# Optimization experiments

Hardware: AMD Instinct MI355X
Metric: run time of the kernel (lower is better)

Reference implementation:

```python
import jax, jax.numpy as jnp
import numpy as np

DIM = 128
WS = 16

def conv2d(x, w, b, padding=0, dilation=1, groups=1):
    out = jax.lax.conv_general_dilated(
        x, w, (1, 1), [(padding, padding), (padding, padding)],
        rhs_dilation=(dilation, dilation),
        dimension_numbers=('NCHW', 'OIHW', 'NCHW'),
        feature_group_count=groups)
    return out + b[None, :, None, None]

def leaky(x):
    return jax.nn.leaky_relu(x, 0.2)

def to_windows(x, ws):
    # [B,C,H,W] -> [B, N, ws*ws*C]  with per-window (dh, dw, c) flatten order
    B, C, H, W = x.shape
    h, w = H // ws, W // ws
    return x.reshape(B, C, h, ws, w, ws).transpose(0, 2, 4, 3, 5, 1).reshape(B, h * w, ws * ws * C)

def from_windows(x, ws, h, w, C):
    B = x.shape[0]
    return x.reshape(B, h, w, ws, ws, C).transpose(0, 5, 1, 3, 2, 4).reshape(B, C, h * ws, w * ws)

def flow_warp(x, flow):
    # bilinear warp with border padding; flow [B,H,W,2] in pixel units (x,y)
    B, C, H, W = x.shape
    gy, gx = jnp.meshgrid(jnp.arange(H, dtype=x.dtype), jnp.arange(W, dtype=x.dtype), indexing='ij')
    sx = jnp.clip(gx[None] + flow[..., 0], 0.0, W - 1.0)
    sy = jnp.clip(gy[None] + flow[..., 1], 0.0, H - 1.0)
    x0 = jnp.floor(sx); y0 = jnp.floor(sy)
    x1 = jnp.clip(x0 + 1.0, 0.0, W - 1.0); y1 = jnp.clip(y0 + 1.0, 0.0, H - 1.0)
    wx = (sx - x0)[:, None]; wy = (sy - y0)[:, None]
    x0i = x0.astype(jnp.int32); x1i = x1.astype(jnp.int32)
    y0i = y0.astype(jnp.int32); y1i = y1.astype(jnp.int32)
    gat = jax.vmap(lambda img, yi, xi: img[:, yi, xi])
    Ia = gat(x, y0i, x0i); Ib = gat(x, y0i, x1i)
    Ic = gat(x, y1i, x0i); Id = gat(x, y1i, x1i)
    return Ia * (1 - wx) * (1 - wy) + Ib * wx * (1 - wy) + Ic * (1 - wx) * wy + Id * wx * wy

def _forward(x, condition_global, gumbel_u, pv_w, pv_b, pq_w, pq_b, pk_w, pk_b,
             cs1_w, cs1_b, cs2_w, cs2_b, cs3_w, cs3_b, po_w, po_b,
             rin_w, rin_b, roff1_w, roff1_b, roff2_w, roff2_b,
             rm1_w, rm1_b, rm2_w, rm2_b, rca_w, rca_b, rsa_w, rsa_b):
    B, C, H, W = x.shape
    ws = WS
    v = conv2d(x, pv_w, pv_b)
    # window coordinate condition, 2 channels
    lin = jnp.linspace(-1.0, 1.0, ws).astype(x.dtype)
    cy, cx = jnp.meshgrid(lin, lin, indexing='ij')
    cond_wind = jnp.tile(jnp.stack([cy, cx])[None], (B, 1, H // ws, W // ws))
    cond = jnp.concatenate([v, condition_global, cond_wind], axis=1)  # [B, C+3, H, W]
    # PredictorLG
    f = leaky(conv2d(cond, rin_w, rin_b))
    offsets = conv2d(leaky(conv2d(f, roff1_w, roff1_b)), roff2_w, roff2_b)  # [B,2,H,W]
    ca = jax.nn.sigmoid(conv2d(f.mean(axis=(2, 3), keepdims=True), rca_w, rca_b))  # [B,C,1,1]
    sa = jax.nn.sigmoid(conv2d(f, rsa_w, rsa_b, padding=1))  # [B,1,H,W]
    mwin = to_windows(f.mean(axis=1, keepdims=True), ws)  # [B,N,ws*ws]
    h1 = leaky(jnp.einsum('bne,oe->bno', mwin, rm1_w) + rm1_b)
    pred = jax.nn.softmax(jnp.einsum('bne,oe->bno', h1, rm2_w) + rm2_b, axis=-1)  # [B,N,2]
    # hard gumbel-softmax with straight-through estimator (tau=1)
    g = -jnp.log(-jnp.log(gumbel_u + 1e-10) + 1e-10)
    y_soft = jax.nn.softmax(pred + g, axis=-1)
    y_hard = jax.nn.one_hot(jnp.argmax(y_soft, -1), 2, dtype=y_soft.dtype)
    mask = (y_hard + y_soft - jax.lax.stop_gradient(y_soft))[:, :, 0:1]  # [B,N,1]
    # flow warp, q=k=warped
    xw = flow_warp(x, offsets.transpose(0, 2, 3, 1))
    qk = jnp.concatenate([xw, xw], axis=1)
    vs = v * sa
    vw = to_windows(v, ws); vsw = to_windows(vs, ws); qkw = to_windows(qk, ws)
    N = vw.shape[1]
    v1 = (vw * mask).reshape(B * N, ws * ws, C)
    v2 = vsw * (1.0 - mask)
    qk1 = (qkw * mask).reshape(B, N * ws * ws, 2 * C)
    q1, k1 = jnp.split(qk1, 2, axis=2)
    q1 = (q1 @ pq_w.T + pq_b).reshape(B * N, ws * ws, C)
    k1 = (k1 @ pk_w.T + pk_b).reshape(B * N, ws * ws, C)
    attn = jax.nn.softmax(q1 @ jnp.swapaxes(k1, -1, -2), axis=-1)  # [B*N, ws^2, ws^2]
    f_attn = (attn @ v1).reshape(B, N, ws * ws * C)
    out = from_windows(f_attn + v2, ws, H // ws, W // ws, C)
    cs = conv2d(out, cs1_w, cs1_b)
    cs = conv2d(cs, cs2_w, cs2_b, padding=2, groups=C)
    cs = conv2d(cs, cs3_w, cs3_b, padding=6, dilation=3, groups=C)
    out = jax.nn.gelu(cs, approximate=False) * ca + out
    return conv2d(out, po_w, po_b)

def setup_inputs() -> dict:
    B, C, H, W, ws = 4, DIM, 256, 256, WS
    cdim = C + 3; c4 = cdim // 4; c8 = cdim // 8
    N = (H // ws) * (W // ws)
    ks = jax.random.split(jax.random.key(0), 20)
    s = 0.05
    def rn(k, shape, scale):
        return jax.random.normal(k, shape, dtype=jnp.float32) * scale
    z = lambda n: jnp.zeros((n,), dtype=jnp.float32)
    return {
        'x': rn(ks[0], (B, C, H, W), 1.0),
        'condition_global': rn(ks[1], (B, 1, H, W), 1.0),
        'gumbel_u': jax.random.uniform(ks[2], (B, N, 2), dtype=jnp.float32, minval=1e-6, maxval=1.0 - 1e-6),
        'pv_w': rn(ks[3], (C, C, 1, 1), s), 'pv_b': z(C),
        'pq_w': rn(ks[4], (C, C), s), 'pq_b': z(C),
        'pk_w': rn(ks[5], (C, C), s), 'pk_b': z(C),
        'cs1_w': rn(ks[6], (C, C, 1, 1), s), 'cs1_b': z(C),
        'cs2_w': rn(ks[7], (C, 1, 5, 5), s), 'cs2_b': z(C),
        'cs3_w': rn(ks[8], (C, 1, 5, 5), s), 'cs3_b': z(C),
        'po_w': rn(ks[9], (C, C, 1, 1), s), 'po_b': z(C),
        'rin_w': rn(ks[10], (c4, cdim, 1, 1), s), 'rin_b': z(c4),
        'roff1_w': rn(ks[11], (c8, c4, 1, 1), s), 'roff1_b': z(c8),
        'roff2_w': rn(ks[12], (2, c8, 1, 1), s), 'roff2_b': z(2),
        'rm1_w': rn(ks[13], (ws, ws * ws), s), 'rm1_b': z(ws),
        'rm2_w': rn(ks[14], (2, ws), s), 'rm2_b': z(2),
        'rca_w': rn(ks[15], (C, c4, 1, 1), s), 'rca_b': z(C),
        'rsa_w': rn(ks[16], (1, c4, 3, 3), s), 'rsa_b': z(1),
    }

def reference(x, condition_global, gumbel_u, pv_w, pv_b, pq_w, pq_b, pk_w, pk_b,
              cs1_w, cs1_b, cs2_w, cs2_b, cs3_w, cs3_b, po_w, po_b,
              rin_w, rin_b, roff1_w, roff1_b, roff2_w, roff2_b,
              rm1_w, rm1_b, rm2_w, rm2_b, rca_w, rca_b, rsa_w, rsa_b):
    return _forward(x, condition_global, gumbel_u, pv_w, pv_b, pq_w, pq_b, pk_w, pk_b,
                    cs1_w, cs1_b, cs2_w, cs2_b, cs3_w, cs3_b, po_w, po_b,
                    rin_w, rin_b, roff1_w, roff1_b, roff2_w, roff2_b,
                    rm1_w, rm1_b, rm2_w, rm2_b, rca_w, rca_b, rsa_w, rsa_b)
```

## Files before the change

### kernel.cpp

```cpp
#include <hip/hip_runtime.h>
#include <hip/hip_bf16.h>


typedef __hip_bfloat16 bf16;
using short8 = __attribute__((ext_vector_type(8))) short;
using f32x4  = __attribute__((ext_vector_type(4))) float;

#define HWP 65536
#define NB  4
#define LB  __launch_bounds__(256)

__device__ __forceinline__ float u2f(unsigned short s) {
    return __uint_as_float(((unsigned int)s) << 16);
}
__device__ __forceinline__ float b2f(bf16 v) { return __bfloat162float(v); }
__device__ __forceinline__ unsigned short f2bu(float x) {
    bf16 h = __float2bfloat16(x);
    return *reinterpret_cast<unsigned short*>(&h);
}
__device__ __forceinline__ float leaky(float x) { return x > 0.f ? x : 0.2f * x; }
__device__ __forceinline__ float sigmoidf(float x) { return 1.f / (1.f + __expf(-x)); }

struct __attribute__((aligned(4))) f2u { float x, y; };

__device__ __forceinline__ void ld8(const float* p, float* f) {
    float4 u0 = *reinterpret_cast<const float4*>(p);
    float4 u1 = *reinterpret_cast<const float4*>(p + 4);
    f[0] = u0.x; f[1] = u0.y; f[2] = u0.z; f[3] = u0.w;
    f[4] = u1.x; f[5] = u1.y; f[6] = u1.z; f[7] = u1.w;
}
__device__ __forceinline__ void ld8(const bf16* p, float* f) {
    uint4 u = *reinterpret_cast<const uint4*>(p);
    const unsigned short* s = reinterpret_cast<const unsigned short*>(&u);
#pragma unroll
    for (int i = 0; i < 8; i++) f[i] = u2f(s[i]);
}
__device__ __forceinline__ void st8(bf16* p, const float* f) {
    uint4 r;
    r.x = (unsigned)f2bu(f[0]) | ((unsigned)f2bu(f[1]) << 16);
    r.y = (unsigned)f2bu(f[2]) | ((unsigned)f2bu(f[3]) << 16);
    r.z = (unsigned)f2bu(f[4]) | ((unsigned)f2bu(f[5]) << 16);
    r.w = (unsigned)f2bu(f[6]) | ((unsigned)f2bu(f[7]) << 16);
    *reinterpret_cast<uint4*>(p) = r;
}
__device__ __forceinline__ void stv4(float* p, float a, float b, float c, float d) {
    float4 v; v.x = a; v.y = b; v.z = c; v.w = d;
    *reinterpret_cast<float4*>(p) = v;
}
__device__ __forceinline__ void stv4(bf16* p, float a, float b, float c, float d) {
    uint2 r;
    r.x = (unsigned)f2bu(a) | ((unsigned)f2bu(b) << 16);
    r.y = (unsigned)f2bu(c) | ((unsigned)f2bu(d) << 16);
    *reinterpret_cast<uint2*>(p) = r;
}

__global__ LB void k_pvconv(const float* __restrict__ in, const float* __restrict__ w,
                            const float* __restrict__ bias, float* __restrict__ out) {
    __shared__ float Wt[32][128];
    __shared__ float Xs[32][64];
    const int tid = threadIdx.x;
    const int p0 = blockIdx.x * 64;
    const int b = blockIdx.y;
    const int pg = tid & 15;
    const int og = tid >> 4;
    float acc[4][8];
#pragma unroll
    for (int i = 0; i < 4; i++)
#pragma unroll
        for (int j = 0; j < 8; j++) acc[i][j] = 0.f;
    const float* inb = in + ((size_t)b * 128) * HWP + p0;
    for (int k0 = 0; k0 < 128; k0 += 32) {
        __syncthreads();
#pragma unroll
        for (int it = 0; it < 4; it++) {
            int jj = tid + it * 256;
            int oc = jj & 127, kq = jj >> 7;
            float4 wv = *reinterpret_cast<const float4*>(w + oc * 128 + k0 + kq * 4);
            Wt[kq * 4 + 0][oc] = wv.x;
            Wt[kq * 4 + 1][oc] = wv.y;
            Wt[kq * 4 + 2][oc] = wv.z;
            Wt[kq * 4 + 3][oc] = wv.w;
        }
        {
            int row = tid >> 3;
            int col0 = (tid & 7) * 8;
            float t8[8];
            ld8(inb + (size_t)(k0 + row) * HWP + col0, t8);
#pragma unroll
            for (int i = 0; i < 8; i++) Xs[row][col0 + i] = t8[i];
        }
        __syncthreads();
#pragma unroll
        for (int kk = 0; kk < 32; kk++) {
            float a0 = Xs[kk][pg * 4 + 0];
            float a1 = Xs[kk][pg * 4 + 1];
            float a2 = Xs[kk][pg * 4 + 2];
            float a3 = Xs[kk][pg * 4 + 3];
            const float* wr = &Wt[kk][og * 8];
#pragma unroll
            for (int j = 0; j < 8; j++) {
                float wv = wr[j];
                acc[0][j] += a0 * wv;
                acc[1][j] += a1 * wv;
                acc[2][j] += a2 * wv;
                acc[3][j] += a3 * wv;
            }
        }
    }
#pragma unroll
    for (int j = 0; j < 8; j++) {
        int oc = og * 8 + j;
        float bv = bias[oc];
        float* po = out + ((size_t)(b * 128 + oc)) * HWP + p0 + pg * 4;
        stv4(po, acc[0][j] + bv, acc[1][j] + bv, acc[2][j] + bv, acc[3][j] + bv);
    }
}

__global__ LB void k_rin(const float* __restrict__ v, const float* __restrict__ cg,
                         const float* __restrict__ w, const float* __restrict__ bias,
                         float* __restrict__ f) {
    __shared__ float Wl[131][36];
    __shared__ float Bs[32];
    const int tid = threadIdx.x;
    for (int i = tid; i < 131 * 32; i += 256) {
        int ic = i >> 5, oc = i & 31;
        Wl[ic][oc] = w[oc * 131 + ic];
    }
    if (tid < 32) Bs[tid] = bias[tid];
    __syncthreads();
    const int p = blockIdx.x * 256 + tid;
    const int b = blockIdx.y;
    float acc[32];
#pragma unroll
    for (int o = 0; o < 32; o++) acc[o] = 0.f;
    const float* vb = v + ((size_t)b * 128) * HWP + p;
    for (int ic = 0; ic < 128; ic++) {
        float a = vb[(size_t)ic * HWP];
#pragma unroll
        for (int o = 0; o < 32; o++) acc[o] += a * Wl[ic][o];
    }
    float a128 = cg[(size_t)b * HWP + p];
    int y = p >> 8, x = p & 255;
    float a129 = -1.f + (2.f / 15.f) * (float)(y & 15);
    float a130 = -1.f + (2.f / 15.f) * (float)(x & 15);
#pragma unroll
    for (int o = 0; o < 32; o++) {
        float r = acc[o] + a128 * Wl[128][o] + a129 * Wl[129][o] + a130 * Wl[130][o] + Bs[o];
        f[((size_t)(b * 32 + o)) * HWP + p] = leaky(r);
    }
}

__global__ LB void k_offsets(const float* __restrict__ f, const float* __restrict__ w1,
                             const float* __restrict__ b1, const float* __restrict__ w2,
                             const float* __restrict__ b2, float* __restrict__ offs) {
    __shared__ float W1[32][16];
    __shared__ float W2[16][2];
    __shared__ float B1[16];
    __shared__ float B2[2];
    const int tid = threadIdx.x;
    for (int i = tid; i < 512; i += 256) {
        int ic = i >> 4, o = i & 15;
        W1[ic][o] = w1[o * 32 + ic];
    }
    if (tid < 32) { int h = tid >> 1, o = tid & 1; W2[h][o] = w2[o * 16 + h]; }
    if (tid < 16) B1[tid] = b1[tid];
    if (tid < 2) B2[tid] = b2[tid];
    __syncthreads();
    const int p = blockIdx.x * 256 + tid;
    const int b = blockIdx.y;
    float h[16];
#pragma unroll
    for (int o = 0; o < 16; o++) h[o] = B1[o];
    for (int ic = 0; ic < 32; ic++) {
        float a = f[((size_t)(b * 32 + ic)) * HWP + p];
#pragma unroll
        for (int o = 0; o < 16; o++) h[o] += a * W1[ic][o];
    }
    float o0 = B2[0], o1 = B2[1];
#pragma unroll
    for (int o = 0; o < 16; o++) {
        float hv = leaky(h[o]);
        o0 += hv * W2[o][0];
        o1 += hv * W2[o][1];
    }
    offs[((size_t)(b * 2 + 0)) * HWP + p] = o0;
    offs[((size_t)(b * 2 + 1)) * HWP + p] = o1;
}

__global__ LB void k_fpix(const float* __restrict__ f, float* __restrict__ fpix) {
    const int p = blockIdx.x * 256 + threadIdx.x;
    const int b = blockIdx.y;
    float s = 0.f;
    for (int c = 0; c < 32; c++) s += f[((size_t)(b * 32 + c)) * HWP + p];
    fpix[(size_t)b * HWP + p] = s * (1.f / 32.f);
}

__global__ LB void k_fmean(const float* __restrict__ f, float* __restrict__ fmean) {
    const int b = blockIdx.x >> 5, c = blockIdx.x & 31;
    const float* base = f + ((size_t)(b * 32 + c)) * HWP;
    float s = 0.f;
    for (int i = threadIdx.x; i < HWP; i += 256) s += base[i];
    __shared__ float red[256];
    red[threadIdx.x] = s;
    __syncthreads();
    for (int st = 128; st > 0; st >>= 1) {
        if (threadIdx.x < st) red[threadIdx.x] += red[threadIdx.x + st];
        __syncthreads();
    }
    if (threadIdx.x == 0) fmean[b * 32 + c] = red[0];
}

__global__ LB void k_ca(const float* __restrict__ fmean, const float* __restrict__ w,
                        const float* __restrict__ bias, float* __restrict__ ca) {
    const int b = blockIdx.x, oc = threadIdx.x;
    float acc = bias[oc];
    for (int ic = 0; ic < 32; ic++)
        acc += w[oc * 32 + ic] * fmean[b * 32 + ic] * (1.f / 65536.f);
    ca[b * 128 + oc] = sigmoidf(acc);
}

__global__ LB void k_sa(const float* __restrict__ f, const float* __restrict__ w,
                        const float* __restrict__ bias, float* __restrict__ sa) {
    __shared__ float Wl[32][9];
    __shared__ float bs;
    const int tid = threadIdx.x;
    for (int i = tid; i < 288; i += 256) Wl[i / 9][i % 9] = w[i];
    if (tid == 0) bs = bias[0];
    __syncthreads();
    const int p = blockIdx.x * 256 + tid;
    const int b = blockIdx.y;
    const int y = p >> 8, x = p & 255;
    float acc = bs;
    for (int ic = 0; ic < 32; ic++) {
        const float* fb = f + ((size_t)(b * 32 + ic)) * HWP;
#pragma unroll
        for (int dy = 0; dy < 3; dy++) {
            int yy = y + dy - 1;
            if ((unsigned)yy >= 256u) continue;
#pragma unroll
            for (int dx = 0; dx < 3; dx++) {
                int xx = x + dx - 1;
                if ((unsigned)xx >= 256u) continue;
                acc += fb[yy * 256 + xx] * Wl[ic][dy * 3 + dx];
            }
        }
    }
    sa[(size_t)b * HWP + p] = sigmoidf(acc);
}

__global__ LB void k_mask(const float* __restrict__ fpix, const float* __restrict__ gum,
                          const float* __restrict__ w1, const float* __restrict__ b1,
                          const float* __restrict__ w2, const float* __restrict__ b2,
                          float* __restrict__ mask) {
    __shared__ float W1[256][16];
    __shared__ float W2[2][16];
    __shared__ float B1[16];
    __shared__ float B2[2];
    const int tid = threadIdx.x;
    for (int i = tid; i < 4096; i += 256) {
        int o = i >> 8, e = i & 255;
        W1[e][o] = w1[o * 256 + e];
    }
    if (tid < 32) W2[tid >> 4][tid & 15] = w2[tid];
    if (tid < 16) B1[tid] = b1[tid];
    if (tid < 2) B2[tid] = b2[tid];
    __syncthreads();
    const int wid = blockIdx.x * 256 + tid;
    const int b = wid >> 8, n = wid & 255;
    const int wy = n >> 4, wx = n & 15;
    const float* fp = fpix + (size_t)b * HWP + (wy * 16) * 256 + wx * 16;
    float h[16];
#pragma unroll
    for (int o = 0; o < 16; o++) h[o] = B1[o];
    for (int e = 0; e < 256; e++) {
        float mv = fp[(e >> 4) * 256 + (e & 15)];
#pragma unroll
        for (int o = 0; o < 16; o++) h[o] += mv * W1[e][o];
    }
    float l0 = B2[0], l1 = B2[1];
#pragma unroll
    for (int o = 0; o < 16; o++) {
        float hv = leaky(h[o]);
        l0 += hv * W2[0][o];
        l1 += hv * W2[1][o];
    }
    float mx = fmaxf(l0, l1);
    float e0 = __expf(l0 - mx), e1 = __expf(l1 - mx);
    float inv = 1.f / (e0 + e1);
    float p0 = e0 * inv, p1 = e1 * inv;
    float u0 = gum[wid * 2 + 0], u1 = gum[wid * 2 + 1];
    float g0 = -logf(-logf(u0 + 1e-10f) + 1e-10f);
    float g1 = -logf(-logf(u1 + 1e-10f) + 1e-10f);
    mask[wid] = (p0 + g0 >= p1 + g1) ? 1.f : 0.f;
}

__global__ LB void k_warp(const float* __restrict__ x, const float* __restrict__ offs,
                          bf16* __restrict__ xw) {
    const int tid = threadIdx.x;
    const int p = blockIdx.x * 64 + (tid & 63);
    const int oct = blockIdx.y * 4 + (tid >> 6);
    const int b = blockIdx.z;
    const int y = p >> 8, xc = p & 255;
    float fx = offs[((size_t)(b * 2 + 0)) * HWP + p];
    float fy = offs[((size_t)(b * 2 + 1)) * HWP + p];
    float sx = fminf(fmaxf((float)xc + fx, 0.f), 255.f);
    float sy = fminf(fmaxf((float)y + fy, 0.f), 255.f);
    int x0 = min((int)sx, 254);
    int y0 = min((int)sy, 254);
    float wx = sx - (float)x0;
    float wy = sy - (float)y0;
    float w00 = (1.f - wx) * (1.f - wy), w01 = wx * (1.f - wy);
    float w10 = (1.f - wx) * wy, w11 = wx * wy;
    const float* base = x + ((size_t)(b * 128 + oct * 8)) * HWP + y0 * 256 + x0;
    float fv[8];
#pragma unroll
    for (int j = 0; j < 8; j++) {
        f2u r0 = *reinterpret_cast<const f2u*>(base + (size_t)j * HWP);
        f2u r1 = *reinterpret_cast<const f2u*>(base + (size_t)j * HWP + 256);
        fv[j] = r0.x * w00 + r0.y * w01 + r1.x * w10 + r1.y * w11;
    }
    const int wid = b * 256 + (y >> 4) * 16 + (xc >> 4);
    const int t = (y & 15) * 16 + (xc & 15);
    st8(xw + ((size_t)(wid * 256 + t)) * 128 + oct * 8, fv);
}

template <int MODE, typename OutT>
__global__ __launch_bounds__(256, 1) void k_wingemm(
        const bf16* __restrict__ A, const float* __restrict__ w,
        const float* __restrict__ bias, const float* __restrict__ mask,
        OutT* __restrict__ outp) {
    const int wid = blockIdx.x;
    if (MODE == 0) {
        if (mask[wid] < 0.5f) return;
    }
    __shared__ unsigned short Wl[128][136];
    __shared__ float Bs[128];
    const int tid = threadIdx.x;
    for (int j = tid; j < 4096; j += 256) {
        int oc = j >> 5, k4 = (j & 31) * 4;
        float4 wv = *reinterpret_cast<const float4*>(w + oc * 128 + k4);
        uint2 r;
        r.x = (unsigned)f2bu(wv.x) | ((unsigned)f2bu(wv.y) << 16);
        r.y = (unsigned)f2bu(wv.z) | ((unsigned)f2bu(wv.w) << 16);
        *reinterpret_cast<uint2*>(&Wl[oc][k4]) = r;
    }
    if (tid < 128) Bs[tid] = bias[tid];
    const int wv_ = tid >> 6, lane = tid & 63, quad = lane >> 4, lid = lane & 15;
    const bf16* arow = A + (size_t)wid * 256 * 128;
    short8 af[4][4];
#pragma unroll
    for (int mt = 0; mt < 4; mt++)
#pragma unroll
        for (int kf = 0; kf < 4; kf++)
            af[mt][kf] = *reinterpret_cast<const short8*>(
                arow + (size_t)(wv_ * 64 + mt * 16 + lid) * 128 + kf * 32 + quad * 8);
    __syncthreads();
    f32x4 acc[4][8];
#pragma unroll
    for (int mt = 0; mt < 4; mt++)
#pragma unroll
        for (int cf = 0; cf < 8; cf++)
#pragma unroll
            for (int i = 0; i < 4; i++) acc[mt][cf][i] = 0.f;
#pragma unroll
    for (int cf = 0; cf < 8; cf++) {
        short8 wf[4];
#pragma unroll
        for (int kf = 0; kf < 4; kf++)
            wf[kf] = *reinterpret_cast<const short8*>(&Wl[cf * 16 + lid][kf * 32 + quad * 8]);
#pragma unroll
        for (int mt = 0; mt < 4; mt++)
#pragma unroll
            for (int kf = 0; kf < 4; kf++)
                acc[mt][cf] = __builtin_amdgcn_mfma_f32_16x16x32_bf16(af[mt][kf], wf[kf], acc[mt][cf], 0, 0, 0);
    }
    if (MODE == 0) {
        bf16* ob = (bf16*)outp;
#pragma unroll
        for (int cf = 0; cf < 8; cf++) {
            float bv = Bs[cf * 16 + lid];
#pragma unroll
            for (int mt = 0; mt < 4; mt++)
#pragma unroll
                for (int i = 0; i < 4; i++) {
                    int row = wv_ * 64 + mt * 16 + quad * 4 + i;
                    *reinterpret_cast<unsigned short*>(
                        &ob[((size_t)(wid * 256 + row)) * 128 + cf * 16 + lid]) =
                        f2bu(acc[mt][cf][i] + bv);
                }
        }
    } else {
        const int b = wid >> 8, n = wid & 255;
        const int wy = n >> 4, wx = n & 15;
#pragma unroll
        for (int cf = 0; cf < 8; cf++) {
            int oc = cf * 16 + lid;
            float bv = Bs[oc];
            OutT* plane = outp + ((size_t)(b * 128 + oc)) * HWP;
#pragma unroll
            for (int mt = 0; mt < 4; mt++) {
                int t0 = wv_ * 64 + mt * 16 + quad * 4;
                int ty = t0 >> 4, tx = t0 & 15;
                int px = (wy * 16 + ty) * 256 + wx * 16 + tx;
                stv4(plane + px, acc[mt][cf][0] + bv, acc[mt][cf][1] + bv,
                     acc[mt][cf][2] + bv, acc[mt][cf][3] + bv);
            }
        }
    }
}

__global__ __launch_bounds__(256, 1) void k_attn(
        const bf16* __restrict__ qbuf, const bf16* __restrict__ kbuf,
        const float* __restrict__ v, const float* __restrict__ sa,
        const float* __restrict__ mask, bf16* __restrict__ wout) {
    const int wid = blockIdx.x;
    const int b = wid >> 8, n = wid & 255;
    const int wy = n >> 4, wx = n & 15;
    const int tid = threadIdx.x;
    const int pixbase = (wy * 16) * 256 + wx * 16;
    const float* vb = v + ((size_t)b * 128) * HWP;
    if (mask[wid] < 0.5f) {
        const int t = tid;
        const int pix = pixbase + (t >> 4) * 256 + (t & 15);
        float s = sa[(size_t)b * HWP + pix];
        bf16* orow = wout + ((size_t)(wid * 256 + t)) * 128;
        for (int c0 = 0; c0 < 128; c0 += 8) {
            float fv[8];
#pragma unroll
            for (int i = 0; i < 8; i++) fv[i] = vb[(size_t)(c0 + i) * HWP + pix] * s;
            st8(orow + c0, fv);
        }
        return;
    }
    __shared__ unsigned short Pl[4][64][72];
    __shared__ unsigned short Vt[128][72];
    const int w = tid >> 6, lane = tid & 63, quad = lane >> 4, lid = lane & 15;
    const bf16* qwin = qbuf + (size_t)wid * 256 * 128;
    const bf16* kwin = kbuf + (size_t)wid * 256 * 128;
    short8 qf[4][4];
#pragma unroll
    for (int mt = 0; mt < 4; mt++)
#pragma unroll
        for (int kf = 0; kf < 4; kf++)
            qf[mt][kf] = *reinterpret_cast<const short8*>(
                qwin + (size_t)(w * 64 + mt * 16 + lid) * 128 + kf * 32 + quad * 8);

    f32x4 O[4][8];
#pragma unroll
    for (int mt = 0; mt < 4; mt++)
#pragma unroll
        for (int cf = 0; cf < 8; cf++)
#pragma unroll
            for (int i = 0; i < 4; i++) O[mt][cf][i] = 0.f;
    float mrow[4][4], lrow[4][4];
#pragma unroll
    for (int mt = 0; mt < 4; mt++)
#pragma unroll
        for (int i = 0; i < 4; i++) { mrow[mt][i] = -1e30f; lrow[mt][i] = 0.f; }

    for (int j0 = 0; j0 < 256; j0 += 64) {
        __syncthreads();
        {
            int c = tid >> 1, jh = (tid & 1) * 32;
            const float* vcol = vb + (size_t)c * HWP + pixbase;
#pragma unroll
            for (int jj = 0; jj < 32; jj += 2) {
                int t1 = j0 + jh + jj, t2 = t1 + 1;
                float v1 = vcol[(t1 >> 4) * 256 + (t1 & 15)];
                float v2 = vcol[(t2 >> 4) * 256 + (t2 & 15)];
                unsigned u = (unsigned)f2bu(v1) | ((unsigned)f2bu(v2) << 16);
                *reinterpret_cast<unsigned*>(&Vt[c][jh + jj]) = u;
            }
        }
        f32x4 sacc[4][4];
#pragma unroll
        for (int nt = 0; nt < 4; nt++) {
            short8 kfr[4];
#pragma unroll
            for (int kf = 0; kf < 4; kf++)
                kfr[kf] = *reinterpret_cast<const short8*>(
                    kwin + (size_t)(j0 + nt * 16 + lid) * 128 + kf * 32 + quad * 8);
#pragma unroll
            for (int mt = 0; mt < 4; mt++) {
                f32x4 acc;
                acc[0] = 0.f; acc[1] = 0.f; acc[2] = 0.f; acc[3] = 0.f;
#pragma unroll
                for (int kf = 0; kf < 4; kf++)
                    acc = __builtin_amdgcn_mfma_f32_16x16x32_bf16(qf[mt][kf], kfr[kf], acc, 0, 0, 0);
                sacc[mt][nt] = acc;
            }
        }
        float alpha[4][4];
#pragma unroll
        for (int mt = 0; mt < 4; mt++)
#pragma unroll
            for (int i = 0; i < 4; i++) {
                float mx = sacc[mt][0][i];
                mx = fmaxf(mx, sacc[mt][1][i]);
                mx = fmaxf(mx, sacc[mt][2][i]);
                mx = fmaxf(mx, sacc[mt][3][i]);
                mx = fmaxf(mx, __shfl_xor(mx, 1));
                mx = fmaxf(mx, __shfl_xor(mx, 2));
                mx = fmaxf(mx, __shfl_xor(mx, 4));
                mx = fmaxf(mx, __shfl_xor(mx, 8));
                float mn = fmaxf(mrow[mt][i], mx);
                alpha[mt][i] = __expf(mrow[mt][i] - mn);
                mrow[mt][i] = mn;
            }
#pragma unroll
        for (int mt = 0; mt < 4; mt++) {
            float ps[4] = {0.f, 0.f, 0.f, 0.f};
#pragma unroll
            for (int nt = 0; nt < 4; nt++)
#pragma unroll
                for (int i = 0; i < 4; i++) {
                    float p = __expf(sacc[mt][nt][i] - mrow[mt][i]);
                    ps[i] += p;
                    Pl[w][mt * 16 + quad * 4 + i][nt * 16 + lid] = f2bu(p);
                }
#pragma unroll
            for (int i = 0; i < 4; i++) {
                float rs = ps[i];
                rs += __shfl_xor(rs, 1);
                rs += __shfl_xor(rs, 2);
                rs += __shfl_xor(rs, 4);
                rs += __shfl_xor(rs, 8);
                lrow[mt][i] = lrow[mt][i] * alpha[mt][i] + rs;
            }
        }
#pragma unroll
        for (int mt = 0; mt < 4; mt++)
#pragma unroll
            for (int cf = 0; cf < 8; cf++)
#pragma unroll
                for (int i = 0; i < 4; i++) O[mt][cf][i] *= alpha[mt][i];
        __syncthreads();
        short8 pa[4][2];
#pragma unroll
        for (int mt = 0; mt < 4; mt++)
#pragma unroll
            for (int kq = 0; kq < 2; kq++)
                pa[mt][kq] = *reinterpret_cast<const short8*>(
                    &Pl[w][mt * 16 + lid][kq * 32 + quad * 8]);
#pragma unroll
        for (int cf = 0; cf < 8; cf++) {
            short8 vf0 = *reinterpret_cast<const short8*>(&Vt[cf * 16 + lid][quad * 8]);
            short8 vf1 = *reinterpret_cast<const short8*>(&Vt[cf * 16 + lid][32 + quad * 8]);
#pragma unroll
            for (int mt = 0; mt < 4; mt++) {
                O[mt][cf] = __builtin_amdgcn_mfma_f32_16x16x32_bf16(pa[mt][0], vf0, O[mt][cf], 0, 0, 0);
                O[mt][cf] = __builtin_amdgcn_mfma_f32_16x16x32_bf16(pa[mt][1], vf1, O[mt][cf], 0, 0, 0);
            }
        }
    }
#pragma unroll
    for (int mt = 0; mt < 4; mt++) {
        float inv[4];
#pragma unroll
        for (int i = 0; i < 4; i++) inv[i] = 1.f / lrow[mt][i];
#pragma unroll
        for (int cf = 0; cf < 8; cf++)
#pragma unroll
            for (int i = 0; i < 4; i++) {
                int row = w * 64 + mt * 16 + quad * 4 + i;
                int col = cf * 16 + lid;
                *reinterpret_cast<unsigned short*>(
                    &wout[((size_t)(wid * 256 + row)) * 128 + col]) = f2bu(O[mt][cf][i] * inv[i]);
            }
    }
}

template <int DIL, bool TOKOUT>
__global__ LB void k_dwconv5(const bf16* __restrict__ in, const float* __restrict__ w,
                             const float* __restrict__ bias, bf16* __restrict__ out) {
    constexpr int HLO = 2 * DIL;
    constexpr int ROWS = 32;
    constexpr int NR = ROWS + 2 * HLO;
    __shared__ unsigned short Ls[NR][272];
    const int tid = threadIdx.x;
    const int bc = blockIdx.y;
    const int c = bc & 127;
    const int r0 = blockIdx.x * ROWS;
    const bf16* ib = in + (size_t)bc * HWP;
    for (int i = tid; i < NR * 32; i += 256) {
        int row = i >> 5, seg = i & 31;
        int y = r0 - HLO + row;
        uint4 val;
        if ((unsigned)y < 256u) {
            val = *reinterpret_cast<const uint4*>(ib + y * 256 + seg * 8);
        } else {
            val.x = 0u; val.y = 0u; val.z = 0u; val.w = 0u;
        }
        *reinterpret_cast<uint4*>(&Ls[row][8 + seg * 8]) = val;
    }
    for (int i = tid; i < NR * 2; i += 256) {
        int row = i >> 1;
        uint4 zz; zz.x = 0u; zz.y = 0u; zz.z = 0u; zz.w = 0u;
        *reinterpret_cast<uint4*>(&Ls[row][(i & 1) ? 264 : 0]) = zz;
    }
    float W[25];
#pragma unroll
    for (int i = 0; i < 25; i++) W[i] = w[c * 25 + i];
    const float bv = bias[c];
    __syncthreads();
    const int x = tid;
    float acc[ROWS];
#pragma unroll
    for (int r = 0; r < ROWS; r++) acc[r] = bv;
#pragma unroll
    for (int iy = 0; iy < NR; iy++) {
        float v5[5];
#pragma unroll
        for (int dx = 0; dx < 5; dx++)
            v5[dx] = u2f(Ls[iy][8 + x + (dx - 2) * DIL]);
#pragma unroll
        for (int dy = 0; dy < 5; dy++) {
            const int ro = iy - HLO + (2 - dy) * DIL;
            if (ro < 0 || ro >= ROWS) continue;
#pragma unroll
            for (int dx = 0; dx < 5; dx++)
                acc[ro] += v5[dx] * W[dy * 5 + dx];
        }
    }
    if (TOKOUT) {
        const int bb = bc >> 7;
#pragma unroll
        for (int r = 0; r < ROWS; r++) {
            int y = r0 + r;
            int wid_ = bb * 256 + (y >> 4) * 16 + (x >> 4);
            int t = (y & 15) * 16 + (x & 15);
            *reinterpret_cast<unsigned short*>(
                &out[((size_t)(wid_ * 256 + t)) * 128 + c]) = f2bu(acc[r]);
        }
    } else {
        bf16* ob = out + (size_t)bc * HWP + (size_t)r0 * 256 + x;
#pragma unroll
        for (int r = 0; r < ROWS; r++)
            *reinterpret_cast<unsigned short*>(&ob[r * 256]) = f2bu(acc[r]);
    }
}

__global__ LB void k_tmp(const bf16* __restrict__ g, const float* __restrict__ ca,
                         const bf16* __restrict__ res, bf16* __restrict__ out) {
    const int i = blockIdx.x * 256 + threadIdx.x;
    const int b = blockIdx.y;
    const int c0 = (i & 15) * 8;
    const size_t base = ((size_t)b * HWP + (i >> 4)) * 128 + c0;
    float gv[8], rv[8], fv[8];
    ld8(g + base, gv);
    ld8(res + base, rv);
    const float* cab = ca + b * 128 + c0;
#pragma unroll
    for (int j = 0; j < 8; j++) {
        float gl = 0.5f * gv[j] * (1.f + erff(gv[j] * 0.70710678118654752f));
        fv[j] = gl * cab[j] + rv[j];
    }
    st8(out + base, fv);
}

extern "C" void kernel_launch(void* const* d_in, const int* in_sizes, int n_in,
                              void* d_out, int out_size, void* d_ws, size_t ws_size,
                              hipStream_t stream) {
    const float* x     = (const float*)d_in[0];
    const float* cg    = (const float*)d_in[1];
    const float* gum   = (const float*)d_in[2];
    const float* pv_w  = (const float*)d_in[3];
    const float* pv_b  = (const float*)d_in[4];
    const float* pq_w  = (const float*)d_in[5];
    const float* pq_b  = (const float*)d_in[6];
    const float* pk_w  = (const float*)d_in[7];
    const float* pk_b  = (const float*)d_in[8];
    const float* cs1_w = (const float*)d_in[9];
    const float* cs1_b = (const float*)d_in[10];
    const float* cs2_w = (const float*)d_in[11];
    const float* cs2_b = (const float*)d_in[12];
    const float* cs3_w = (const float*)d_in[13];
    const float* cs3_b = (const float*)d_in[14];
    const float* po_w  = (const float*)d_in[15];
    const float* po_b  = (const float*)d_in[16];
    const float* rin_w = (const float*)d_in[17];
    const float* rin_b = (const float*)d_in[18];
    const float* ro1_w = (const float*)d_in[19];
    const float* ro1_b = (const float*)d_in[20];
    const float* ro2_w = (const float*)d_in[21];
    const float* ro2_b = (const float*)d_in[22];
    const float* rm1_w = (const float*)d_in[23];
    const float* rm1_b = (const float*)d_in[24];
    const float* rm2_w = (const float*)d_in[25];
    const float* rm2_b = (const float*)d_in[26];
    const float* rca_w = (const float*)d_in[27];
    const float* rca_b = (const float*)d_in[28];
    const float* rsa_w = (const float*)d_in[29];
    const float* rsa_b = (const float*)d_in[30];

    char* wsp = (char*)d_ws;
    size_t off = 0;
    auto alloc = [&](size_t bytes) -> char* {
        char* p = wsp + off;
        off += (bytes + 255) & ~(size_t)255;
        return p;
    };
    const size_t NELT = (size_t)NB * 128 * HWP;
    float* v    = (float*)alloc(NELT * 4);
    float* f    = (float*)alloc((size_t)NB * 32 * HWP * 4);
    bf16*  xw   = (bf16*)alloc(NELT * 2);
    bf16*  qb   = (bf16*)alloc(NELT * 2);
    bf16*  kb   = (bf16*)alloc(NELT * 2);
    float* offs = (float*)alloc((size_t)NB * 2 * HWP * 4);
    float* sab  = (float*)alloc((size_t)NB * HWP * 4);
    float* fpix = (float*)alloc((size_t)NB * HWP * 4);
    float* fmean= (float*)alloc(NB * 32 * 4);
    float* cab  = (float*)alloc(NB * 128 * 4);
    float* mk   = (float*)alloc(NB * 256 * 4);
    bf16*  dw1o = (bf16*)v;
    (void)ws_size; (void)in_sizes; (void)n_in; (void)out_size;

    float* out = (float*)d_out;
    dim3 gpix(256, NB);

    k_pvconv<<<dim3(1024, NB), 256, 0, stream>>>(x, pv_w, pv_b, v);
    k_rin<<<gpix, 256, 0, stream>>>(v, cg, rin_w, rin_b, f);
    k_offsets<<<gpix, 256, 0, stream>>>(f, ro1_w, ro1_b, ro2_w, ro2_b, offs);
    k_fpix<<<gpix, 256, 0, stream>>>(f, fpix);
    k_fmean<<<dim3(NB * 32), 256, 0, stream>>>(f, fmean);
    k_ca<<<dim3(NB), 128, 0, stream>>>(fmean, rca_w, rca_b, cab);
    k_sa<<<gpix, 256, 0, stream>>>(f, rsa_w, rsa_b, sab);
    k_mask<<<dim3(NB), 256, 0, stream>>>(fpix, gum, rm1_w, rm1_b, rm2_w, rm2_b, mk);
    k_warp<<<dim3(1024, 4, NB), 256, 0, stream>>>(x, offs, xw);
    k_wingemm<0, bf16><<<dim3(NB * 256), 256, 0, stream>>>(xw, pq_w, pq_b, mk, qb);
    k_wingemm<0, bf16><<<dim3(NB * 256), 256, 0, stream>>>(xw, pk_w, pk_b, mk, kb);
    k_attn<<<dim3(NB * 256), 256, 0, stream>>>(qb, kb, v, sab, mk, xw);
    k_wingemm<1, bf16><<<dim3(NB * 256), 256, 0, stream>>>(xw, cs1_w, cs1_b, mk, kb);
    k_dwconv5<1, false><<<dim3(256 / 32, NB * 128), 256, 0, stream>>>(kb, cs2_w, cs2_b, dw1o);
    k_dwconv5<3, true><<<dim3(256 / 32, NB * 128), 256, 0, stream>>>(dw1o, cs3_w, cs3_b, qb);
    k_tmp<<<dim3(4096, NB), 256, 0, stream>>>(qb, cab, xw, kb);
    k_wingemm<2, float><<<dim3(NB * 256), 256, 0, stream>>>(kb, po_w, po_b, mk, out);
}
```

Baseline: 1.256 ms.

## Emit windowed bf16 V layout from pvconv and fuse fpix into offsets

The pointwise V convolution now also writes a per-window, channel-major bf16 copy of V. The attention kernel reads its MFMA V fragments straight from global memory instead of gathering fp32 V into shared memory and converting it every tile, which also removes the per-tile block barriers. Separately, the per-pixel channel mean is accumulated inside the offsets kernel, so one kernel launch and one full read of f go away. The cost is an extra bf16 buffer of V-tensor size, extra writes in pvconv, and uncached global reads in the attention inner loop.

```diff
diff --git a/kernel.cpp b/kernel.cpp
--- a/kernel.cpp
+++ b/kernel.cpp
@@ -55,7 +55,8 @@
 }
 
 __global__ LB void k_pvconv(const float* __restrict__ in, const float* __restrict__ w,
-                            const float* __restrict__ bias, float* __restrict__ out) {
+                            const float* __restrict__ bias, float* __restrict__ out,
+                            bf16* __restrict__ vt) {
     __shared__ float Wt[32][128];
     __shared__ float Xs[32][64];
     const int tid = threadIdx.x;
@@ -107,12 +108,19 @@
             }
         }
     }
+    const int y = p0 >> 8;
+    const int xbase = (p0 & 255) + pg * 4;
+    const int wid = b * 256 + (y >> 4) * 16 + (xbase >> 4);
+    const int t0 = (y & 15) * 16 + (xbase & 15);
 #pragma unroll
     for (int j = 0; j < 8; j++) {
         int oc = og * 8 + j;
         float bv = bias[oc];
+        float r0 = acc[0][j] + bv, r1 = acc[1][j] + bv;
+        float r2 = acc[2][j] + bv, r3 = acc[3][j] + bv;
         float* po = out + ((size_t)(b * 128 + oc)) * HWP + p0 + pg * 4;
-        stv4(po, acc[0][j] + bv, acc[1][j] + bv, acc[2][j] + bv, acc[3][j] + bv);
+        stv4(po, r0, r1, r2, r3);
+        stv4(vt + ((size_t)wid * 128 + oc) * 256 + t0, r0, r1, r2, r3);
     }
 }
 
@@ -152,7 +160,8 @@
 
 __global__ LB void k_offsets(const float* __restrict__ f, const float* __restrict__ w1,
                              const float* __restrict__ b1, const float* __restrict__ w2,
-                             const float* __restrict__ b2, float* __restrict__ offs) {
+                             const float* __restrict__ b2, float* __restrict__ offs,
+                             float* __restrict__ fpix) {
     __shared__ float W1[32][16];
     __shared__ float W2[16][2];
     __shared__ float B1[16];
@@ -171,8 +180,10 @@
     float h[16];
 #pragma unroll
     for (int o = 0; o < 16; o++) h[o] = B1[o];
+    float s = 0.f;
     for (int ic = 0; ic < 32; ic++) {
         float a = f[((size_t)(b * 32 + ic)) * HWP + p];
+        s += a;
 #pragma unroll
         for (int o = 0; o < 16; o++) h[o] += a * W1[ic][o];
     }
@@ -185,13 +196,6 @@
     }
     offs[((size_t)(b * 2 + 0)) * HWP + p] = o0;
     offs[((size_t)(b * 2 + 1)) * HWP + p] = o1;
-}
-
-__global__ LB void k_fpix(const float* __restrict__ f, float* __restrict__ fpix) {
-    const int p = blockIdx.x * 256 + threadIdx.x;
-    const int b = blockIdx.y;
-    float s = 0.f;
-    for (int c = 0; c < 32; c++) s += f[((size_t)(b * 32 + c)) * HWP + p];
     fpix[(size_t)b * HWP + p] = s * (1.f / 32.f);
 }
 
@@ -411,15 +415,16 @@
 
 __global__ __launch_bounds__(256, 1) void k_attn(
         const bf16* __restrict__ qbuf, const bf16* __restrict__ kbuf,
-        const float* __restrict__ v, const float* __restrict__ sa,
-        const float* __restrict__ mask, bf16* __restrict__ wout) {
+        const bf16* __restrict__ vt, const float* __restrict__ v,
+        const float* __restrict__ sa, const float* __restrict__ mask,
+        bf16* __restrict__ wout) {
     const int wid = blockIdx.x;
     const int b = wid >> 8, n = wid & 255;
     const int wy = n >> 4, wx = n & 15;
     const int tid = threadIdx.x;
     const int pixbase = (wy * 16) * 256 + wx * 16;
-    const float* vb = v + ((size_t)b * 128) * HWP;
     if (mask[wid] < 0.5f) {
+        const float* vb = v + ((size_t)b * 128) * HWP;
         const int t = tid;
         const int pix = pixbase + (t >> 4) * 256 + (t & 15);
         float s = sa[(size_t)b * HWP + pix];
@@ -433,10 +438,10 @@
         return;
     }
     __shared__ unsigned short Pl[4][64][72];
-    __shared__ unsigned short Vt[128][72];
     const int w = tid >> 6, lane = tid & 63, quad = lane >> 4, lid = lane & 15;
     const bf16* qwin = qbuf + (size_t)wid * 256 * 128;
     const bf16* kwin = kbuf + (size_t)wid * 256 * 128;
+    const bf16* vtw = vt + (size_t)wid * 128 * 256;
     short8 qf[4][4];
 #pragma unroll
     for (int mt = 0; mt < 4; mt++)
@@ -459,19 +464,6 @@
         for (int i = 0; i < 4; i++) { mrow[mt][i] = -1e30f; lrow[mt][i] = 0.f; }
 
     for (int j0 = 0; j0 < 256; j0 += 64) {
-        __syncthreads();
-        {
-            int c = tid >> 1, jh = (tid & 1) * 32;
-            const float* vcol = vb + (size_t)c * HWP + pixbase;
-#pragma unroll
-            for (int jj = 0; jj < 32; jj += 2) {
-                int t1 = j0 + jh + jj, t2 = t1 + 1;
-                float v1 = vcol[(t1 >> 4) * 256 + (t1 & 15)];
-                float v2 = vcol[(t2 >> 4) * 256 + (t2 & 15)];
-                unsigned u = (unsigned)f2bu(v1) | ((unsigned)f2bu(v2) << 16);
-                *reinterpret_cast<unsigned*>(&Vt[c][jh + jj]) = u;
-            }
-        }
         f32x4 sacc[4][4];
 #pragma unroll
         for (int nt = 0; nt < 4; nt++) {
@@ -534,7 +526,8 @@
             for (int cf = 0; cf < 8; cf++)
 #pragma unroll
                 for (int i = 0; i < 4; i++) O[mt][cf][i] *= alpha[mt][i];
-        __syncthreads();
+        asm volatile("s_waitcnt lgkmcnt(0)" ::: "memory");
+        __builtin_amdgcn_sched_barrier(0);
         short8 pa[4][2];
 #pragma unroll
         for (int mt = 0; mt < 4; mt++)
@@ -544,14 +537,17 @@
                     &Pl[w][mt * 16 + lid][kq * 32 + quad * 8]);
 #pragma unroll
         for (int cf = 0; cf < 8; cf++) {
-            short8 vf0 = *reinterpret_cast<const short8*>(&Vt[cf * 16 + lid][quad * 8]);
-            short8 vf1 = *reinterpret_cast<const short8*>(&Vt[cf * 16 + lid][32 + quad * 8]);
+            const bf16* vr = vtw + (size_t)(cf * 16 + lid) * 256 + j0 + quad * 8;
+            short8 vf0 = *reinterpret_cast<const short8*>(vr);
+            short8 vf1 = *reinterpret_cast<const short8*>(vr + 32);
 #pragma unroll
             for (int mt = 0; mt < 4; mt++) {
                 O[mt][cf] = __builtin_amdgcn_mfma_f32_16x16x32_bf16(pa[mt][0], vf0, O[mt][cf], 0, 0, 0);
                 O[mt][cf] = __builtin_amdgcn_mfma_f32_16x16x32_bf16(pa[mt][1], vf1, O[mt][cf], 0, 0, 0);
             }
         }
+        asm volatile("s_waitcnt lgkmcnt(0)" ::: "memory");
+        __builtin_amdgcn_sched_barrier(0);
     }
 #pragma unroll
     for (int mt = 0; mt < 4; mt++) {
@@ -703,6 +699,7 @@
     const size_t NELT = (size_t)NB * 128 * HWP;
     float* v    = (float*)alloc(NELT * 4);
     float* f    = (float*)alloc((size_t)NB * 32 * HWP * 4);
+    bf16*  vt   = (bf16*)alloc(NELT * 2);
     bf16*  xw   = (bf16*)alloc(NELT * 2);
     bf16*  qb   = (bf16*)alloc(NELT * 2);
     bf16*  kb   = (bf16*)alloc(NELT * 2);
@@ -718,10 +715,9 @@
     float* out = (float*)d_out;
     dim3 gpix(256, NB);
 
-    k_pvconv<<<dim3(1024, NB), 256, 0, stream>>>(x, pv_w, pv_b, v);
+    k_pvconv<<<dim3(1024, NB), 256, 0, stream>>>(x, pv_w, pv_b, v, vt);
     k_rin<<<gpix, 256, 0, stream>>>(v, cg, rin_w, rin_b, f);
-    k_offsets<<<gpix, 256, 0, stream>>>(f, ro1_w, ro1_b, ro2_w, ro2_b, offs);
-    k_fpix<<<gpix, 256, 0, stream>>>(f, fpix);
+    k_offsets<<<gpix, 256, 0, stream>>>(f, ro1_w, ro1_b, ro2_w, ro2_b, offs, fpix);
     k_fmean<<<dim3(NB * 32), 256, 0, stream>>>(f, fmean);
     k_ca<<<dim3(NB), 128, 0, stream>>>(fmean, rca_w, rca_b, cab);
     k_sa<<<gpix, 256, 0, stream>>>(f, rsa_w, rsa_b, sab);
@@ -729,7 +725,7 @@
     k_warp<<<dim3(1024, 4, NB), 256, 0, stream>>>(x, offs, xw);
     k_wingemm<0, bf16><<<dim3(NB * 256), 256, 0, stream>>>(xw, pq_w, pq_b, mk, qb);
     k_wingemm<0, bf16><<<dim3(NB * 256), 256, 0, stream>>>(xw, pk_w, pk_b, mk, kb);
-    k_attn<<<dim3(NB * 256), 256, 0, stream>>>(qb, kb, v, sab, mk, xw);
+    k_attn<<<dim3(NB * 256), 256, 0, stream>>>(qb, kb, vt, v, sab, mk, xw);
     k_wingemm<1, bf16><<<dim3(NB * 256), 256, 0, stream>>>(xw, cs1_w, cs1_b, mk, kb);
     k_dwconv5<1, false><<<dim3(256 / 32, NB * 128), 256, 0, stream>>>(kb, cs2_w, cs2_b, dw1o);
     k_dwconv5<3, true><<<dim3(256 / 32, NB * 128), 256, 0, stream>>>(dw1o, cs3_w, cs3_b, qb);
```

Measured after the change: 1.330 ms. +6.0%, slower.

## Pre-transpose V windows to bf16 and fuse fpix into offsets kernel

Applied to the files above, without the earlier changes.

Adds a kernel that converts each masked window of V into a contiguous bf16 channel-major tile, so the attention kernel fills its shared V tile with 16-byte vector copies. This replaces strided fp32 gathers and conversions inside the attention loop. It also folds the per-pixel channel mean into the offsets kernel, which already reads f, and drops the separate fpix launch. The cost is an extra launch and an extra workspace buffer written and re-read.

```diff
diff --git a/kernel.cpp b/kernel.cpp
--- a/kernel.cpp
+++ b/kernel.cpp
@@ -116,6 +116,29 @@
     }
 }
 
+__global__ LB void k_vtr(const float* __restrict__ v, const float* __restrict__ mask,
+                         bf16* __restrict__ vt) {
+    const int wid = blockIdx.x;
+    if (mask[wid] < 0.5f) return;
+    const int b = wid >> 8, n = wid & 255;
+    const int wy = n >> 4, wx = n & 15;
+    const float* vb = v + ((size_t)b * 128) * HWP + (wy * 16) * 256 + wx * 16;
+    bf16* vw = vt + (size_t)wid * 128 * 256;
+    const int y16 = threadIdx.x & 15;
+    const int oc0 = threadIdx.x >> 4;
+#pragma unroll
+    for (int g = 0; g < 8; g++) {
+        int oc = g * 16 + oc0;
+        const float* src = vb + (size_t)oc * HWP + y16 * 256;
+        float ta[8], tb[8];
+        ld8(src, ta);
+        ld8(src + 8, tb);
+        bf16* dst = vw + oc * 256 + y16 * 16;
+        st8(dst, ta);
+        st8(dst + 8, tb);
+    }
+}
+
 __global__ LB void k_rin(const float* __restrict__ v, const float* __restrict__ cg,
                          const float* __restrict__ w, const float* __restrict__ bias,
                          float* __restrict__ f) {
@@ -152,7 +175,8 @@
 
 __global__ LB void k_offsets(const float* __restrict__ f, const float* __restrict__ w1,
                              const float* __restrict__ b1, const float* __restrict__ w2,
-                             const float* __restrict__ b2, float* __restrict__ offs) {
+                             const float* __restrict__ b2, float* __restrict__ offs,
+                             float* __restrict__ fpix) {
     __shared__ float W1[32][16];
     __shared__ float W2[16][2];
     __shared__ float B1[16];
@@ -171,8 +195,10 @@
     float h[16];
 #pragma unroll
     for (int o = 0; o < 16; o++) h[o] = B1[o];
+    float s = 0.f;
     for (int ic = 0; ic < 32; ic++) {
         float a = f[((size_t)(b * 32 + ic)) * HWP + p];
+        s += a;
 #pragma unroll
         for (int o = 0; o < 16; o++) h[o] += a * W1[ic][o];
     }
@@ -185,13 +211,6 @@
     }
     offs[((size_t)(b * 2 + 0)) * HWP + p] = o0;
     offs[((size_t)(b * 2 + 1)) * HWP + p] = o1;
-}
-
-__global__ LB void k_fpix(const float* __restrict__ f, float* __restrict__ fpix) {
-    const int p = blockIdx.x * 256 + threadIdx.x;
-    const int b = blockIdx.y;
-    float s = 0.f;
-    for (int c = 0; c < 32; c++) s += f[((size_t)(b * 32 + c)) * HWP + p];
     fpix[(size_t)b * HWP + p] = s * (1.f / 32.f);
 }
 
@@ -411,15 +430,16 @@
 
 __global__ __launch_bounds__(256, 1) void k_attn(
         const bf16* __restrict__ qbuf, const bf16* __restrict__ kbuf,
-        const float* __restrict__ v, const float* __restrict__ sa,
-        const float* __restrict__ mask, bf16* __restrict__ wout) {
+        const bf16* __restrict__ vt, const float* __restrict__ v,
+        const float* __restrict__ sa, const float* __restrict__ mask,
+        bf16* __restrict__ wout) {
     const int wid = blockIdx.x;
     const int b = wid >> 8, n = wid & 255;
     const int wy = n >> 4, wx = n & 15;
     const int tid = threadIdx.x;
     const int pixbase = (wy * 16) * 256 + wx * 16;
-    const float* vb = v + ((size_t)b * 128) * HWP;
     if (mask[wid] < 0.5f) {
+        const float* vb = v + ((size_t)b * 128) * HWP;
         const int t = tid;
         const int pix = pixbase + (t >> 4) * 256 + (t & 15);
         float s = sa[(size_t)b * HWP + pix];
@@ -437,6 +457,7 @@
     const int w = tid >> 6, lane = tid & 63, quad = lane >> 4, lid = lane & 15;
     const bf16* qwin = qbuf + (size_t)wid * 256 * 128;
     const bf16* kwin = kbuf + (size_t)wid * 256 * 128;
+    const bf16* vtw = vt + (size_t)wid * 128 * 256;
     short8 qf[4][4];
 #pragma unroll
     for (int mt = 0; mt < 4; mt++)
@@ -462,15 +483,12 @@
         __syncthreads();
         {
             int c = tid >> 1, jh = (tid & 1) * 32;
-            const float* vcol = vb + (size_t)c * HWP + pixbase;
-#pragma unroll
-            for (int jj = 0; jj < 32; jj += 2) {
-                int t1 = j0 + jh + jj, t2 = t1 + 1;
-                float v1 = vcol[(t1 >> 4) * 256 + (t1 & 15)];
-                float v2 = vcol[(t2 >> 4) * 256 + (t2 & 15)];
-                unsigned u = (unsigned)f2bu(v1) | ((unsigned)f2bu(v2) << 16);
-                *reinterpret_cast<unsigned*>(&Vt[c][jh + jj]) = u;
-            }
+            const uint4* src = reinterpret_cast<const uint4*>(vtw + (size_t)c * 256 + j0 + jh);
+            uint4* dst = reinterpret_cast<uint4*>(&Vt[c][jh]);
+            dst[0] = src[0];
+            dst[1] = src[1];
+            dst[2] = src[2];
+            dst[3] = src[3];
         }
         f32x4 sacc[4][4];
 #pragma unroll
@@ -703,6 +721,7 @@
     const size_t NELT = (size_t)NB * 128 * HWP;
     float* v    = (float*)alloc(NELT * 4);
     float* f    = (float*)alloc((size_t)NB * 32 * HWP * 4);
+    bf16*  vt   = (bf16*)alloc(NELT * 2);
     bf16*  xw   = (bf16*)alloc(NELT * 2);
     bf16*  qb   = (bf16*)alloc(NELT * 2);
     bf16*  kb   = (bf16*)alloc(NELT * 2);
@@ -720,16 +739,16 @@
 
     k_pvconv<<<dim3(1024, NB), 256, 0, stream>>>(x, pv_w, pv_b, v);
     k_rin<<<gpix, 256, 0, stream>>>(v, cg, rin_w, rin_b, f);
-    k_offsets<<<gpix, 256, 0, stream>>>(f, ro1_w, ro1_b, ro2_w, ro2_b, offs);
-    k_fpix<<<gpix, 256, 0, stream>>>(f, fpix);
+    k_offsets<<<gpix, 256, 0, stream>>>(f, ro1_w, ro1_b, ro2_w, ro2_b, offs, fpix);
     k_fmean<<<dim3(NB * 32), 256, 0, stream>>>(f, fmean);
     k_ca<<<dim3(NB), 128, 0, stream>>>(fmean, rca_w, rca_b, cab);
     k_sa<<<gpix, 256, 0, stream>>>(f, rsa_w, rsa_b, sab);
     k_mask<<<dim3(NB), 256, 0, stream>>>(fpix, gum, rm1_w, rm1_b, rm2_w, rm2_b, mk);
+    k_vtr<<<dim3(NB * 256), 256, 0, stream>>>(v, mk, vt);
     k_warp<<<dim3(1024, 4, NB), 256, 0, stream>>>(x, offs, xw);
     k_wingemm<0, bf16><<<dim3(NB * 256), 256, 0, stream>>>(xw, pq_w, pq_b, mk, qb);
     k_wingemm<0, bf16><<<dim3(NB * 256), 256, 0, stream>>>(xw, pk_w, pk_b, mk, kb);
-    k_attn<<<dim3(NB * 256), 256, 0, stream>>>(qb, kb, v, sab, mk, xw);
+    k_attn<<<dim3(NB * 256), 256, 0, stream>>>(qb, kb, vt, v, sab, mk, xw);
     k_wingemm<1, bf16><<<dim3(NB * 256), 256, 0, stream>>>(xw, cs1_w, cs1_b, mk, kb);
     k_dwconv5<1, false><<<dim3(256 / 32, NB * 128), 256, 0, stream>>>(kb, cs2_w, cs2_b, dw1o);
     k_dwconv5<3, true><<<dim3(256 / 32, NB * 128), 256, 0, stream>>>(dw1o, cs3_w, cs3_b, qb);
```

Measured after the change: 1.264 ms. No clear change (+0.7%).
